# Optimization experiments

Measured on AMD Instinct MI355X. Metric: run time of the kernel, lower is better.

The kernel has to match this reference:

```python
import jax, jax.numpy as jnp
import numpy as np

D_MODEL = 512
HEADS = 8
HEAD_DIM = D_MODEL // HEADS
LN_EPS = 1e-5


def _rel_shift(pos_score):
    # pos_score: [B, H, T, P] with P = 2T-1
    B, H, T, P = pos_score.shape
    padded = jnp.pad(pos_score, ((0, 0), (0, 0), (0, 0), (1, 0)))  # [B,H,T,P+1]
    shifted = padded.reshape(B, H, P + 1, T)[:, :, 1:, :].reshape(B, H, T, P)
    return shifted[:, :, :, : P // 2 + 1]  # [B,H,T,T]


def setup_inputs() -> dict:
    key = jax.random.key(0)
    ks = jax.random.split(key, 16)
    B, T = 16, 512
    P = 2 * T - 1
    s = 1.0 / np.sqrt(D_MODEL)
    inp = {
        "x": jax.random.normal(ks[0], (B, T, D_MODEL), jnp.float32),
        "pos_emb": jax.random.normal(ks[1], (B, P, D_MODEL), jnp.float32),
        "ln_g": jnp.ones((D_MODEL,), jnp.float32),
        "ln_b": jnp.zeros((D_MODEL,), jnp.float32),
        "Wq": jax.random.normal(ks[2], (D_MODEL, D_MODEL), jnp.float32) * s,
        "bq": jnp.zeros((D_MODEL,), jnp.float32),
        "Wk": jax.random.normal(ks[3], (D_MODEL, D_MODEL), jnp.float32) * s,
        "bk": jnp.zeros((D_MODEL,), jnp.float32),
        "Wv": jax.random.normal(ks[4], (D_MODEL, D_MODEL), jnp.float32) * s,
        "bv": jnp.zeros((D_MODEL,), jnp.float32),
        "Wp": jax.random.normal(ks[5], (D_MODEL, D_MODEL), jnp.float32) * s,
        "bp": jnp.zeros((D_MODEL,), jnp.float32),
        "content_bias": jax.random.normal(ks[6], (HEADS, HEAD_DIM), jnp.float32) * 0.05,
        "position_bias": jax.random.normal(ks[7], (HEADS, HEAD_DIM), jnp.float32) * 0.05,
        "Wo": jax.random.normal(ks[8], (D_MODEL, D_MODEL), jnp.float32) * s,
        "bo": jnp.zeros((D_MODEL,), jnp.float32),
    }
    return inp


def reference(x, pos_emb, ln_g, ln_b, Wq, bq, Wk, bk, Wv, bv, Wp, bp,
              content_bias, position_bias, Wo, bo):
    B, T, D = x.shape
    H, hd = HEADS, HEAD_DIM

    # LayerNorm over last dim
    mu = jnp.mean(x, axis=-1, keepdims=True)
    var = jnp.var(x, axis=-1, keepdims=True)
    xn = (x - mu) / jnp.sqrt(var + LN_EPS) * ln_g + ln_b

    q = (xn @ Wq.T + bq).reshape(B, T, H, hd)                 # [B,T,H,hd]
    k = (xn @ Wk.T + bk).reshape(B, T, H, hd)                 # [B,T,H,hd]
    v = (xn @ Wv.T + bv).reshape(B, T, H, hd)                 # [B,T,H,hd]
    p = (pos_emb @ Wp.T + bp).reshape(B, -1, H, hd)           # [B,P,H,hd]

    content_score = jnp.einsum('bshd,bthd->bhst', q + content_bias, k)   # [B,H,T,T]
    pos_score = jnp.einsum('bshd,bphd->bhsp', q + position_bias, p)      # [B,H,T,P]
    pos_score = _rel_shift(pos_score)                                    # [B,H,T,T]

    scores = (content_score + pos_score) / jnp.sqrt(jnp.asarray(hd, x.dtype))
    w = jax.nn.softmax(scores, axis=-1)
    ctx = jnp.einsum('bhst,bthd->bshd', w, v).reshape(B, T, D)
    return ctx @ Wo.T + bo
```

## Files before the change

### kernel.cpp

```cpp
#include <hip/hip_runtime.h>
#include <cstdio>
#include <cstdint>


typedef short s16x8 __attribute__((ext_vector_type(8)));
typedef float f32x4 __attribute__((ext_vector_type(4)));
typedef unsigned short u16x4 __attribute__((ext_vector_type(4)));
typedef unsigned short u16x8 __attribute__((ext_vector_type(8)));

#define CSCALE 0.1803368801111204f

#if __has_builtin(__builtin_amdgcn_exp2f)
#define EXP2(x) __builtin_amdgcn_exp2f(x)
#else
#define EXP2(x) exp2f(x)
#endif

__device__ __forceinline__ unsigned short f2bf(float f) {
  unsigned int u = __builtin_bit_cast(unsigned int, f);
  unsigned int r = (u + 0x7FFFu + ((u >> 16) & 1u)) >> 16;
  return (unsigned short)r;
}
__device__ __forceinline__ float bf2f(unsigned short h) {
  unsigned int u = ((unsigned int)h) << 16;
  return __builtin_bit_cast(float, u);
}
__device__ __forceinline__ size_t pk(int row, int col) {
  return (size_t)(row >> 4) * 8192 + (col >> 5) * 512 + ((col >> 3) & 3) * 128 +
         (row & 15) * 8 + (col & 7);
}

__device__ __forceinline__ void gload_lds16(const unsigned short* g,
                                            unsigned short* l) {
  __builtin_amdgcn_global_load_lds(
      (const __attribute__((address_space(1))) unsigned int*)g,
      (__attribute__((address_space(3))) unsigned int*)l, 16, 0, 0);
}

__global__ __launch_bounds__(256) void megaprep(
    const float* __restrict__ x, const float* __restrict__ g,
    const float* __restrict__ bb, unsigned short* __restrict__ xpk,
    const float* __restrict__ pe, unsigned short* __restrict__ pepk,
    const float* __restrict__ Wq, const float* __restrict__ Wk,
    const float* __restrict__ Wp, const float* __restrict__ Wv,
    const float* __restrict__ Wo, const float* __restrict__ bq,
    const float* __restrict__ bk, unsigned short* __restrict__ wqk,
    unsigned short* __restrict__ wpm, unsigned short* __restrict__ wvm,
    unsigned short* __restrict__ wom, float* __restrict__ bqk) {
  const int bid = blockIdx.x, tid = threadIdx.x;
  if (bid < 2048) {
    const int wave = tid >> 6, lane = tid & 63;
    const int row = bid * 4 + wave;
    const int c0 = lane * 8;
    const float* xr = x + (size_t)row * 512 + c0;
    float4 v0 = *(const float4*)xr;
    float4 v1 = *(const float4*)(xr + 4);
    float vv[8] = {v0.x, v0.y, v0.z, v0.w, v1.x, v1.y, v1.z, v1.w};
    float s = 0.f, ss = 0.f;
#pragma unroll
    for (int j = 0; j < 8; ++j) { s += vv[j]; ss += vv[j] * vv[j]; }
#pragma unroll
    for (int d = 1; d < 64; d <<= 1) {
      s += __shfl_xor(s, d, 64);
      ss += __shfl_xor(ss, d, 64);
    }
    const float mu = s * (1.0f / 512.0f);
    const float var = ss * (1.0f / 512.0f) - mu * mu;
    const float rstd = rsqrtf(var + 1e-5f);
    u16x8 o;
#pragma unroll
    for (int j = 0; j < 8; ++j)
      o[j] = f2bf((vv[j] - mu) * rstd * g[c0 + j] + bb[c0 + j]);
    *(u16x8*)(xpk + pk(row, c0)) = o;
  } else if (bid < 6144) {
    int gid = (bid - 2048) * 256 + tid;
    int e = gid * 8;
    int r = e >> 9, c = e & 511;
    int b = r >> 10, u = r & 1023;
    u16x8 o = {0, 0, 0, 0, 0, 0, 0, 0};
    if (u < 1023) {
      const float* src = pe + (size_t)(b * 1023 + u) * 512 + c;
      float4 v0 = *(const float4*)src;
      float4 v1 = *(const float4*)(src + 4);
      o[0] = f2bf(v0.x); o[1] = f2bf(v0.y); o[2] = f2bf(v0.z); o[3] = f2bf(v0.w);
      o[4] = f2bf(v1.x); o[5] = f2bf(v1.y); o[6] = f2bf(v1.z); o[7] = f2bf(v1.w);
    }
    *(u16x8*)(pepk + (size_t)b * 524288 + pk(u, c)) = o;
  } else {
    int gid = (bid - 6144) * 256 + tid;
    int idx = gid * 8;
    int region = idx >> 18, off = idx & 262143;
    const float* src = (region == 0)   ? Wq
                       : (region == 1) ? Wk
                       : (region == 2) ? Wp
                       : (region == 3) ? Wv
                                       : Wo;
    float4 v0 = *(const float4*)(src + off);
    float4 v1 = *(const float4*)(src + off + 4);
    u16x8 o;
    o[0] = f2bf(v0.x); o[1] = f2bf(v0.y); o[2] = f2bf(v0.z); o[3] = f2bf(v0.w);
    o[4] = f2bf(v1.x); o[5] = f2bf(v1.y); o[6] = f2bf(v1.z); o[7] = f2bf(v1.w);
    int n = off >> 9, k = off & 511;
    unsigned short* dst;
    int nrow = n;
    if (region == 0) { dst = wqk; }
    else if (region == 1) { dst = wqk; nrow = n + 512; }
    else if (region == 2) { dst = wpm; }
    else if (region == 3) { dst = wvm; }
    else { dst = wom; }
    *(u16x8*)(dst + pk(nrow, k)) = o;
    if (idx < 1024) {
#pragma unroll
      for (int j = 0; j < 8; j++) {
        int ii = idx + j;
        bqk[ii] = (ii < 512) ? bq[ii] : bk[ii - 512];
      }
    }
  }
}

__device__ __forceinline__ void strip_gemm(
    const unsigned short* __restrict__ Apk, int astrip4,
    const unsigned short* __restrict__ Bpk, int bstrip4,
    unsigned short* __restrict__ lA, int wave, int lane, f32x4 acc[4][4]) {
  {
    const unsigned short* ga =
        Apk + (size_t)(astrip4 + wave) * 8192 + lane * 8;
    unsigned short* la = lA + wave * 8192;
#pragma unroll
    for (int i = 0; i < 16; ++i) gload_lds16(ga + i * 512, la + i * 512);
  }
  __syncthreads();

  const unsigned short* lrd = lA + lane * 8;
  const unsigned short* gb = Bpk + (size_t)bstrip4 * 8192 + lane * 8;
  s16x8 af[2][4], bf[2][4];
#pragma unroll
  for (int mt = 0; mt < 4; ++mt) af[0][mt] = *(const s16x8*)(lrd + mt * 8192);
#pragma unroll
  for (int nt = 0; nt < 4; ++nt)
    bf[0][nt] = *(const s16x8*)(gb + (size_t)nt * 8192);
#pragma unroll
  for (int kc = 0; kc < 16; ++kc) {
    const int cur = kc & 1, nxt = cur ^ 1;
    if (kc < 15) {
#pragma unroll
      for (int mt = 0; mt < 4; ++mt)
        af[nxt][mt] = *(const s16x8*)(lrd + mt * 8192 + (kc + 1) * 512);
#pragma unroll
      for (int nt = 0; nt < 4; ++nt)
        bf[nxt][nt] = *(const s16x8*)(gb + (size_t)nt * 8192 + (kc + 1) * 512);
    }
#pragma unroll
    for (int mt = 0; mt < 4; ++mt)
#pragma unroll
      for (int nt = 0; nt < 4; ++nt)
        acc[mt][nt] = __builtin_amdgcn_mfma_f32_16x16x32_bf16(
            af[cur][mt], bf[cur][nt], acc[cur ? mt : mt][nt], 0, 0, 0);
  }
}

__global__ __launch_bounds__(256) void proj_all(
    const unsigned short* __restrict__ xpk, const unsigned short* __restrict__ pepk,
    const unsigned short* __restrict__ wqk, const unsigned short* __restrict__ wpm,
    const unsigned short* __restrict__ wvm, const float* __restrict__ bqk,
    const float* __restrict__ bp, const float* __restrict__ bv,
    const float* __restrict__ cbv, const float* __restrict__ pbv,
    unsigned short* __restrict__ qc, unsigned short* __restrict__ qp,
    unsigned short* __restrict__ kb, unsigned short* __restrict__ pbuf,
    unsigned short* __restrict__ vth) {
  __shared__ __align__(16) unsigned short lA[32768];
  const int tid = threadIdx.x, lane = tid & 63, wave = tid >> 6;
  const int bid = blockIdx.x;
  const int fr = lane & 15, hi2 = lane >> 4;
  f32x4 fz = {0.f, 0.f, 0.f, 0.f};
  f32x4 acc[4][4];
#pragma unroll
  for (int i = 0; i < 4; i++)
#pragma unroll
    for (int j = 0; j < 4; j++) acc[i][j] = fz;

  if (bid < 512) {
    int strip = bid >> 2, cg = bid & 3;
    int m0 = strip * 64, n0 = cg * 256 + wave * 64;
    strip_gemm(xpk, strip * 4, wqk, n0 >> 4, lA, wave, lane, acc);
#pragma unroll
    for (int nt = 0; nt < 4; ++nt) {
      int col = n0 + nt * 16 + fr;
      float bval = bqk[col];
#pragma unroll
      for (int mt = 0; mt < 4; ++mt) {
        int row = m0 + mt * 16 + hi2 * 4;
        int b = row >> 9, s15 = row & 15, s16i = (row & 511) >> 4;
        if (col < 512) {
          int h = col >> 6, cc = col & 63;
          size_t idx = ((size_t)(b * 8 + h) * 32 + s16i) * 1024 +
                       (cc >> 5) * 512 + ((cc & 31) >> 3) * 128 + (cc & 7);
          float cbc = cbv[col], pbc = pbv[col];
#pragma unroll
          for (int r = 0; r < 4; ++r) {
            float val = acc[mt][nt][r] + bval;
            qc[idx + (s15 + r) * 8] = f2bf((val + cbc) * CSCALE);
            qp[idx + (s15 + r) * 8] = f2bf((val + pbc) * CSCALE);
          }
        } else {
          int c2 = col - 512, h = c2 >> 6, cc = c2 & 63;
          size_t idx = ((size_t)(b * 8 + h) * 32 + s16i) * 1024 +
                       (cc >> 5) * 512 + ((cc & 31) >> 3) * 128 + (cc & 7);
#pragma unroll
          for (int r = 0; r < 4; ++r)
            kb[idx + (s15 + r) * 8] = f2bf(acc[mt][nt][r] + bval);
        }
      }
    }
  } else if (bid < 1024) {
    int pid = bid - 512;
    int b = pid >> 5, rem = pid & 31;
    int strip16 = rem >> 1, cg = rem & 1;
    int u0 = strip16 * 64, n0 = cg * 256 + wave * 64;
    strip_gemm(pepk + (size_t)b * 524288, strip16 * 4, wpm, n0 >> 4, lA, wave,
               lane, acc);
#pragma unroll
    for (int nt = 0; nt < 4; ++nt) {
      int col = n0 + nt * 16 + fr;
      float bval = bp[col];
      int h = col >> 6, cc = col & 63;
      size_t cbase = (size_t)(b * 8 + h) * 64 * 1024 + (cc >> 5) * 512 +
                     ((cc & 31) >> 3) * 128 + (cc & 7);
#pragma unroll
      for (int mt = 0; mt < 4; ++mt) {
        int ub = u0 + mt * 16 + hi2 * 4;
#pragma unroll
        for (int r = 0; r < 4; ++r) {
          int u = ub + r;
          float val = (u >= 1023) ? 0.f : (acc[mt][nt][r] + bval);
          pbuf[cbase + (size_t)(u >> 4) * 1024 + (u & 15) * 8] = f2bf(val);
        }
      }
    }
  } else {
    int vid = bid - 1024;
    int strip = vid >> 1, cg = vid & 1;
    int m0 = strip * 64, n0 = cg * 256 + wave * 64;
    strip_gemm(xpk, strip * 4, wvm, n0 >> 4, lA, wave, lane, acc);
#pragma unroll
    for (int nt = 0; nt < 4; ++nt) {
      int col = n0 + nt * 16 + fr;
      float bval = bv[col];
      int h = col >> 6, d = col & 63;
#pragma unroll
      for (int mt = 0; mt < 4; ++mt) {
        int rowb = m0 + mt * 16 + hi2 * 4;
        int b = rowb >> 9, t = rowb & 511;
        size_t idx = ((size_t)((b * 8 + h) * 4 + (d >> 4)) * 16 + (t >> 5)) * 512 +
                     ((t & 31) >> 3) * 128 + (d & 15) * 8 + (t & 7);
        u16x4 hv;
#pragma unroll
        for (int r = 0; r < 4; ++r) hv[r] = f2bf(acc[mt][nt][r] + bval);
        *(u16x4*)(vth + idx) = hv;
      }
    }
  }
}

__global__ __launch_bounds__(256) void out_gemm(
    const unsigned short* __restrict__ ctxpk, const unsigned short* __restrict__ wom,
    const float* __restrict__ bo, float* __restrict__ out) {
  __shared__ __align__(16) unsigned short lA[32768];
  const int tid = threadIdx.x, lane = tid & 63, wave = tid >> 6;
  const int bid = blockIdx.x;
  const int fr = lane & 15, hi2 = lane >> 4;
  int strip = bid >> 1, cg = bid & 1;
  int m0 = strip * 64, n0 = cg * 256 + wave * 64;
  f32x4 fz = {0.f, 0.f, 0.f, 0.f};
  f32x4 acc[4][4];
#pragma unroll
  for (int i = 0; i < 4; i++)
#pragma unroll
    for (int j = 0; j < 4; j++) acc[i][j] = fz;
  strip_gemm(ctxpk, strip * 4, wom, n0 >> 4, lA, wave, lane, acc);
#pragma unroll
  for (int nt = 0; nt < 4; ++nt) {
    int col = n0 + nt * 16 + fr;
    float bval = bo[col];
#pragma unroll
    for (int mt = 0; mt < 4; ++mt) {
      int row = m0 + mt * 16 + hi2 * 4;
#pragma unroll
      for (int r = 0; r < 4; ++r)
        out[(size_t)(row + r) * 512 + col] = acc[mt][nt][r] + bval;
    }
  }
}

__global__ __launch_bounds__(256) void flash_attn(
    const unsigned short* __restrict__ qc, const unsigned short* __restrict__ qp,
    const unsigned short* __restrict__ kb, const unsigned short* __restrict__ pm,
    const unsigned short* __restrict__ vth, unsigned short* __restrict__ ctxpk) {
  const int id = blockIdx.x;
  const int bh = id & 127, b = bh >> 3, h = bh & 7;
  const int s_blk = id >> 7;
  const int tid = threadIdx.x, wave = tid >> 6, lane = tid & 63;
  const int fr = lane & 15, hi2 = lane >> 4, fc = hi2 * 8;
  const int s0w = s_blk * 64 + wave * 16;
  const int crow = hi2 * 4;

  __shared__ __align__(16) unsigned short Ph_s[4][16][40];
  unsigned short(*Phw)[40] = Ph_s[wave];

  int srcl[4];
#pragma unroll
  for (int r = 0; r < 4; ++r) srcl[r] = (hi2 << 4) | ((fr - (crow + r) - 1) & 15);

  const size_t qtb = ((size_t)(b * 8 + h) * 32 + (s0w >> 4)) * 1024 + lane * 8;
  s16x8 aqc0 = *(const s16x8*)(qc + qtb);
  s16x8 aqc1 = *(const s16x8*)(qc + qtb + 512);
  s16x8 aqp0 = *(const s16x8*)(qp + qtb);
  s16x8 aqp1 = *(const s16x8*)(qp + qtb + 512);

  const unsigned short* kpk = kb + (size_t)(b * 8 + h) * 32 * 1024 + lane * 8;
  const unsigned short* ppk = pm + (size_t)(b * 8 + h) * 64 * 1024 + lane * 8;
  const unsigned short* vhk = vth + (size_t)(b * 8 + h) * 64 * 512 + lane * 8;

  f32x4 fz = {0.f, 0.f, 0.f, 0.f};
  f32x4 Oacc[4] = {fz, fz, fz, fz};
  float lsum[4] = {0.f, 0.f, 0.f, 0.f};

  s16x8 kfA[4], pfA[6], vfA[4], kfB[4], pfB[6], vfB[4];

#define LOADF(step, kf, pf, vf)                                              \
  {                                                                          \
    const int t0_ = (step) * 32;                                             \
    const int u0w_ = t0_ - s0w + 496;                                        \
    const int kt_ = t0_ >> 4, ut_ = u0w_ >> 4, vt_ = t0_ >> 5;               \
    _Pragma("unroll") for (int nt = 0; nt < 2; ++nt) {                       \
      const unsigned short* kr = kpk + (size_t)(kt_ + nt) * 1024;            \
      kf[2 * nt] = *(const s16x8*)kr;                                        \
      kf[2 * nt + 1] = *(const s16x8*)(kr + 512);                            \
    }                                                                        \
    _Pragma("unroll") for (int nt = 0; nt < 3; ++nt) {                       \
      const unsigned short* pr = ppk + (size_t)(ut_ + nt) * 1024;            \
      pf[2 * nt] = *(const s16x8*)pr;                                        \
      pf[2 * nt + 1] = *(const s16x8*)(pr + 512);                            \
    }                                                                        \
    _Pragma("unroll") for (int nt = 0; nt < 4; ++nt)                         \
        vf[nt] = *(const s16x8*)(vhk + (size_t)(nt * 16 + vt_) * 512);       \
  }

#define STEPF(kf, pf, vf)                                                    \
  {                                                                          \
    f32x4 sc[2] = {fz, fz};                                                  \
    _Pragma("unroll") for (int nt = 0; nt < 2; ++nt) {                       \
      sc[nt] = __builtin_amdgcn_mfma_f32_16x16x32_bf16(aqc0, kf[2 * nt],     \
                                                       sc[nt], 0, 0, 0);     \
      sc[nt] = __builtin_amdgcn_mfma_f32_16x16x32_bf16(aqc1, kf[2 * nt + 1], \
                                                       sc[nt], 0, 0, 0);     \
    }                                                                        \
    f32x4 sp[3];                                                             \
    _Pragma("unroll") for (int nt = 0; nt < 3; ++nt) {                       \
      f32x4 t = fz;                                                          \
      t = __builtin_amdgcn_mfma_f32_16x16x32_bf16(aqp0, pf[2 * nt], t, 0, 0, 0); \
      t = __builtin_amdgcn_mfma_f32_16x16x32_bf16(aqp1, pf[2 * nt + 1], t, 0, 0, 0); \
      sp[nt] = t;                                                            \
    }                                                                        \
    float sj[3][4];                                                          \
    _Pragma("unroll") for (int j = 0; j < 3; ++j)                            \
        _Pragma("unroll") for (int r = 0; r < 4; ++r)                        \
        sj[j][r] = __shfl(sp[j][r], srcl[r], 64);                            \
    _Pragma("unroll") for (int nt = 0; nt < 2; ++nt) {                       \
      int tc = nt * 16 + fr;                                                 \
      _Pragma("unroll") for (int r = 0; r < 4; ++r) {                        \
        float pos = (fr <= crow + r) ? sj[nt][r] : sj[nt + 1][r];            \
        float e = EXP2(sc[nt][r] + pos);                                     \
        lsum[r] += e;                                                        \
        Phw[crow + r][tc] = f2bf(e);                                         \
      }                                                                      \
    }                                                                        \
    s16x8 ah = *(const s16x8*)&Phw[fr][fc];                                  \
    _Pragma("unroll") for (int nt = 0; nt < 4; ++nt)                         \
        Oacc[nt] = __builtin_amdgcn_mfma_f32_16x16x32_bf16(ah, vf[nt],       \
                                                           Oacc[nt], 0, 0, 0); \
  }

  LOADF(0, kfA, pfA, vfA);
  for (int s2 = 0; s2 < 8; ++s2) {
    LOADF(2 * s2 + 1, kfB, pfB, vfB);
    STEPF(kfA, pfA, vfA);
    if (s2 < 7) LOADF(2 * s2 + 2, kfA, pfA, vfA);
    STEPF(kfB, pfB, vfB);
  }
#undef LOADF
#undef STEPF

#pragma unroll
  for (int d = 1; d < 16; d <<= 1)
#pragma unroll
    for (int r = 0; r < 4; ++r) lsum[r] += __shfl_xor(lsum[r], d, 64);
#pragma unroll
  for (int nt = 0; nt < 4; ++nt)
#pragma unroll
    for (int r = 0; r < 4; ++r) {
      float o = Oacc[nt][r] / lsum[r];
      int row = b * 512 + s0w + crow + r;
      int col = h * 64 + nt * 16 + fr;
      ctxpk[pk(row, col)] = f2bf(o);
    }
}

extern "C" void kernel_launch(void* const* d_in, const int* in_sizes, int n_in,
                              void* d_out, int out_size, void* d_ws,
                              size_t ws_size, hipStream_t stream) {
  const float* x = (const float*)d_in[0];
  const float* pe = (const float*)d_in[1];
  const float* ln_g = (const float*)d_in[2];
  const float* ln_b = (const float*)d_in[3];
  const float* Wq = (const float*)d_in[4];
  const float* bq = (const float*)d_in[5];
  const float* Wk = (const float*)d_in[6];
  const float* bk = (const float*)d_in[7];
  const float* Wv = (const float*)d_in[8];
  const float* bv = (const float*)d_in[9];
  const float* Wp = (const float*)d_in[10];
  const float* bp = (const float*)d_in[11];
  const float* cb = (const float*)d_in[12];
  const float* pb = (const float*)d_in[13];
  const float* Wo = (const float*)d_in[14];
  const float* bo = (const float*)d_in[15];
  float* out = (float*)d_out;

  char* ws = (char*)d_ws;
  size_t off = 0;
  auto alloc = [&](size_t bytes) -> char* {
    char* ptr = ws + off;
    off = (off + bytes + 255) & ~(size_t)255;
    return ptr;
  };
  unsigned short* xpk = (unsigned short*)alloc((size_t)8192 * 512 * 2);
  unsigned short* ctxpk = xpk;
  unsigned short* pepk = (unsigned short*)alloc((size_t)16384 * 512 * 2);
  unsigned short* vt_hi = (unsigned short*)alloc((size_t)8192 * 512 * 2);
  unsigned short* wqk = (unsigned short*)alloc((size_t)1024 * 512 * 2);
  unsigned short* wpm = (unsigned short*)alloc((size_t)512 * 512 * 2);
  unsigned short* wvm = (unsigned short*)alloc((size_t)512 * 512 * 2);
  unsigned short* wom = (unsigned short*)alloc((size_t)512 * 512 * 2);
  float* bqk = (float*)alloc(1024 * 4);
  unsigned short* qc = (unsigned short*)alloc((size_t)8192 * 512 * 2);
  unsigned short* qp = (unsigned short*)alloc((size_t)8192 * 512 * 2);
  unsigned short* kbuf = (unsigned short*)alloc((size_t)8192 * 512 * 2);
  unsigned short* pbuf = (unsigned short*)alloc((size_t)16384 * 512 * 2);

  if (ws_size < off) {
    fprintf(stderr, "kernel_launch: ws too small (need %zu, have %zu)\n", off,
            ws_size);
    return;
  }

  megaprep<<<6784, 256, 0, stream>>>(x, ln_g, ln_b, xpk, pe, pepk, Wq, Wk, Wp,
                                     Wv, Wo, bq, bk, wqk, wpm, wvm, wom, bqk);
  proj_all<<<1280, 256, 0, stream>>>(xpk, pepk, wqk, wpm, wvm, bqk, bp, bv,
                                     cb, pb, qc, qp, kbuf, pbuf, vt_hi);
  flash_attn<<<1024, 256, 0, stream>>>(qc, qp, kbuf, pbuf, vt_hi, ctxpk);
  out_gemm<<<256, 256, 0, stream>>>(ctxpk, wom, bo, out);
}
```

Measured before the change: 213.5 us.

## Swap MFMA operands for vectorized epilogue stores and triple-buffer B loads

Adds a template flag to the strip GEMM that swaps the MFMA A/B operands, so each lane's accumulator holds four consecutive output columns instead of four rows. The QK, positional and output-projection epilogues then write packed 4-element bf16 or float4 stores and load the biases as float4, replacing scattered scalar stores. It also deepens the global B-fragment prefetch from double to triple buffering to hide more load latency. The extra buffer adds register pressure, and the V path keeps the old operand order.

New measurement: 214.8 us. Within noise of the previous version (+0.6%).

```diff
diff --git a/kernel.cpp b/kernel.cpp
--- a/kernel.cpp
+++ b/kernel.cpp
@@ -119,6 +119,7 @@
   }
 }
 
+template <bool SWAP>
 __device__ __forceinline__ void strip_gemm(
     const unsigned short* __restrict__ Apk, int astrip4,
     const unsigned short* __restrict__ Bpk, int bstrip4,
@@ -134,29 +135,37 @@
 
   const unsigned short* lrd = lA + lane * 8;
   const unsigned short* gb = Bpk + (size_t)bstrip4 * 8192 + lane * 8;
-  s16x8 af[2][4], bf[2][4];
+  s16x8 af[2][4], bf[3][4];
 #pragma unroll
   for (int mt = 0; mt < 4; ++mt) af[0][mt] = *(const s16x8*)(lrd + mt * 8192);
 #pragma unroll
-  for (int nt = 0; nt < 4; ++nt)
+  for (int nt = 0; nt < 4; ++nt) {
     bf[0][nt] = *(const s16x8*)(gb + (size_t)nt * 8192);
+    bf[1][nt] = *(const s16x8*)(gb + (size_t)nt * 8192 + 512);
+  }
 #pragma unroll
   for (int kc = 0; kc < 16; ++kc) {
-    const int cur = kc & 1, nxt = cur ^ 1;
+    if (kc < 14) {
+#pragma unroll
+      for (int nt = 0; nt < 4; ++nt)
+        bf[(kc + 2) % 3][nt] =
+            *(const s16x8*)(gb + (size_t)nt * 8192 + (kc + 2) * 512);
+    }
     if (kc < 15) {
 #pragma unroll
       for (int mt = 0; mt < 4; ++mt)
-        af[nxt][mt] = *(const s16x8*)(lrd + mt * 8192 + (kc + 1) * 512);
+        af[(kc + 1) & 1][mt] =
+            *(const s16x8*)(lrd + mt * 8192 + (kc + 1) * 512);
+    }
+#pragma unroll
+    for (int mt = 0; mt < 4; ++mt)
 #pragma unroll
       for (int nt = 0; nt < 4; ++nt)
-        bf[nxt][nt] = *(const s16x8*)(gb + (size_t)nt * 8192 + (kc + 1) * 512);
-    }
-#pragma unroll
-    for (int mt = 0; mt < 4; ++mt)
-#pragma unroll
-      for (int nt = 0; nt < 4; ++nt)
-        acc[mt][nt] = __builtin_amdgcn_mfma_f32_16x16x32_bf16(
-            af[cur][mt], bf[cur][nt], acc[cur ? mt : mt][nt], 0, 0, 0);
+        acc[mt][nt] =
+            SWAP ? __builtin_amdgcn_mfma_f32_16x16x32_bf16(
+                       bf[kc % 3][nt], af[kc & 1][mt], acc[mt][nt], 0, 0, 0)
+                 : __builtin_amdgcn_mfma_f32_16x16x32_bf16(
+                       af[kc & 1][mt], bf[kc % 3][nt], acc[mt][nt], 0, 0, 0);
   }
 }
 
@@ -183,33 +192,48 @@
   if (bid < 512) {
     int strip = bid >> 2, cg = bid & 3;
     int m0 = strip * 64, n0 = cg * 256 + wave * 64;
-    strip_gemm(xpk, strip * 4, wqk, n0 >> 4, lA, wave, lane, acc);
+    strip_gemm<true>(xpk, strip * 4, wqk, n0 >> 4, lA, wave, lane, acc);
 #pragma unroll
     for (int nt = 0; nt < 4; ++nt) {
-      int col = n0 + nt * 16 + fr;
-      float bval = bqk[col];
-#pragma unroll
-      for (int mt = 0; mt < 4; ++mt) {
-        int row = m0 + mt * 16 + hi2 * 4;
-        int b = row >> 9, s15 = row & 15, s16i = (row & 511) >> 4;
-        if (col < 512) {
-          int h = col >> 6, cc = col & 63;
-          size_t idx = ((size_t)(b * 8 + h) * 32 + s16i) * 1024 +
-                       (cc >> 5) * 512 + ((cc & 31) >> 3) * 128 + (cc & 7);
-          float cbc = cbv[col], pbc = pbv[col];
+      int colb = n0 + nt * 16 + hi2 * 4;
+      float4 b4 = *(const float4*)(bqk + colb);
+      float bvv[4] = {b4.x, b4.y, b4.z, b4.w};
+      if (colb < 512) {
+        int h = colb >> 6, cc = colb & 63;
+        float4 c4 = *(const float4*)(cbv + colb);
+        float4 p4 = *(const float4*)(pbv + colb);
+        float cvv[4] = {c4.x, c4.y, c4.z, c4.w};
+        float pvv[4] = {p4.x, p4.y, p4.z, p4.w};
+        size_t cpart = (size_t)(cc >> 5) * 512 + ((cc & 31) >> 3) * 128 +
+                       (cc & 7) + (size_t)h * 32768;
+#pragma unroll
+        for (int mt = 0; mt < 4; ++mt) {
+          int row = m0 + mt * 16 + fr;
+          int b = row >> 9, s16i = (row & 511) >> 4;
+          size_t idx = ((size_t)b * 8 * 32 + s16i) * 1024 + cpart + fr * 8;
+          u16x4 oc, op;
 #pragma unroll
           for (int r = 0; r < 4; ++r) {
-            float val = acc[mt][nt][r] + bval;
-            qc[idx + (s15 + r) * 8] = f2bf((val + cbc) * CSCALE);
-            qp[idx + (s15 + r) * 8] = f2bf((val + pbc) * CSCALE);
+            float val = acc[mt][nt][r] + bvv[r];
+            oc[r] = f2bf((val + cvv[r]) * CSCALE);
+            op[r] = f2bf((val + pvv[r]) * CSCALE);
           }
-        } else {
-          int c2 = col - 512, h = c2 >> 6, cc = c2 & 63;
-          size_t idx = ((size_t)(b * 8 + h) * 32 + s16i) * 1024 +
-                       (cc >> 5) * 512 + ((cc & 31) >> 3) * 128 + (cc & 7);
-#pragma unroll
-          for (int r = 0; r < 4; ++r)
-            kb[idx + (s15 + r) * 8] = f2bf(acc[mt][nt][r] + bval);
+          *(u16x4*)(qc + idx) = oc;
+          *(u16x4*)(qp + idx) = op;
+        }
+      } else {
+        int c2 = colb - 512, h = c2 >> 6, cc = c2 & 63;
+        size_t cpart = (size_t)(cc >> 5) * 512 + ((cc & 31) >> 3) * 128 +
+                       (cc & 7) + (size_t)h * 32768;
+#pragma unroll
+        for (int mt = 0; mt < 4; ++mt) {
+          int row = m0 + mt * 16 + fr;
+          int b = row >> 9, s16i = (row & 511) >> 4;
+          size_t idx = ((size_t)b * 8 * 32 + s16i) * 1024 + cpart + fr * 8;
+          u16x4 ok;
+#pragma unroll
+          for (int r = 0; r < 4; ++r) ok[r] = f2bf(acc[mt][nt][r] + bvv[r]);
+          *(u16x4*)(kb + idx) = ok;
         }
       }
     }
@@ -218,31 +242,35 @@
     int b = pid >> 5, rem = pid & 31;
     int strip16 = rem >> 1, cg = rem & 1;
     int u0 = strip16 * 64, n0 = cg * 256 + wave * 64;
-    strip_gemm(pepk + (size_t)b * 524288, strip16 * 4, wpm, n0 >> 4, lA, wave,
-               lane, acc);
+    strip_gemm<true>(pepk + (size_t)b * 524288, strip16 * 4, wpm, n0 >> 4, lA,
+                     wave, lane, acc);
 #pragma unroll
     for (int nt = 0; nt < 4; ++nt) {
-      int col = n0 + nt * 16 + fr;
-      float bval = bp[col];
-      int h = col >> 6, cc = col & 63;
-      size_t cbase = (size_t)(b * 8 + h) * 64 * 1024 + (cc >> 5) * 512 +
+      int colb = n0 + nt * 16 + hi2 * 4;
+      float4 b4 = *(const float4*)(bp + colb);
+      float bvv[4] = {b4.x, b4.y, b4.z, b4.w};
+      int h = colb >> 6, cc = colb & 63;
+      size_t cbase = (size_t)(b * 8 + h) * 65536 + (cc >> 5) * 512 +
                      ((cc & 31) >> 3) * 128 + (cc & 7);
 #pragma unroll
       for (int mt = 0; mt < 4; ++mt) {
-        int ub = u0 + mt * 16 + hi2 * 4;
-#pragma unroll
-        for (int r = 0; r < 4; ++r) {
-          int u = ub + r;
-          float val = (u >= 1023) ? 0.f : (acc[mt][nt][r] + bval);
-          pbuf[cbase + (size_t)(u >> 4) * 1024 + (u & 15) * 8] = f2bf(val);
+        int u = u0 + mt * 16 + fr;
+        size_t idx = cbase + (size_t)(u >> 4) * 1024 + (u & 15) * 8;
+        u16x4 o;
+        if (u >= 1023) {
+          o[0] = 0; o[1] = 0; o[2] = 0; o[3] = 0;
+        } else {
+#pragma unroll
+          for (int r = 0; r < 4; ++r) o[r] = f2bf(acc[mt][nt][r] + bvv[r]);
         }
+        *(u16x4*)(pbuf + idx) = o;
       }
     }
   } else {
     int vid = bid - 1024;
     int strip = vid >> 1, cg = vid & 1;
     int m0 = strip * 64, n0 = cg * 256 + wave * 64;
-    strip_gemm(xpk, strip * 4, wvm, n0 >> 4, lA, wave, lane, acc);
+    strip_gemm<false>(xpk, strip * 4, wvm, n0 >> 4, lA, wave, lane, acc);
 #pragma unroll
     for (int nt = 0; nt < 4; ++nt) {
       int col = n0 + nt * 16 + fr;
@@ -278,17 +306,20 @@
   for (int i = 0; i < 4; i++)
 #pragma unroll
     for (int j = 0; j < 4; j++) acc[i][j] = fz;
-  strip_gemm(ctxpk, strip * 4, wom, n0 >> 4, lA, wave, lane, acc);
+  strip_gemm<true>(ctxpk, strip * 4, wom, n0 >> 4, lA, wave, lane, acc);
 #pragma unroll
   for (int nt = 0; nt < 4; ++nt) {
-    int col = n0 + nt * 16 + fr;
-    float bval = bo[col];
+    int colb = n0 + nt * 16 + hi2 * 4;
+    float4 b4 = *(const float4*)(bo + colb);
 #pragma unroll
     for (int mt = 0; mt < 4; ++mt) {
-      int row = m0 + mt * 16 + hi2 * 4;
-#pragma unroll
-      for (int r = 0; r < 4; ++r)
-        out[(size_t)(row + r) * 512 + col] = acc[mt][nt][r] + bval;
+      int row = m0 + mt * 16 + fr;
+      float4 o;
+      o.x = acc[mt][nt][0] + b4.x;
+      o.y = acc[mt][nt][1] + b4.y;
+      o.z = acc[mt][nt][2] + b4.z;
+      o.w = acc[mt][nt][3] + b4.w;
+      *(float4*)(out + (size_t)row * 512 + colb) = o;
     }
   }
 }
```
